# Kernel tuning notes

Measured on AMD Instinct MI355X. Metric: run time of the kernel, lower is better.

The kernel has to match this reference:

```python
import jax, jax.numpy as jnp
import numpy as np

M, N, D = 512, 4096, 128
H = N // D  # 32
L = 4096   # cache length


def setup_inputs() -> dict:
    key = jax.random.key(0)
    ks = jax.random.split(key, 6)
    s = 1.0 / np.sqrt(N)
    return {
        "X": jax.random.normal(ks[0], (M, N), jnp.float32),
        "W_q": jax.random.normal(ks[1], (N, N), jnp.float32) * s,
        "W_k": jax.random.normal(ks[2], (N, N), jnp.float32) * s,
        "W_v": jax.random.normal(ks[3], (N, N), jnp.float32) * s,
        "cache_K": jax.random.normal(ks[4], (H, L, D), jnp.float32),
        "cache_V": jax.random.normal(ks[5], (H, L, D), jnp.float32),
        "P": 3584,
    }


def reference(X, W_q, W_k, W_v, cache_K, cache_V, P):
    # nn.Linear(N, N, bias=False): y = x @ W.T
    q = (X @ W_q.T).reshape(M, H, D).transpose(1, 0, 2)  # [H, M, D]
    k = (X @ W_k.T).reshape(M, H, D).transpose(1, 0, 2)  # [H, M, D]
    v = (X @ W_v.T).reshape(M, H, D).transpose(1, 0, 2)  # [H, M, D]
    # KV-cache write at position P (static slice under jit for fixed P)
    cK = jax.lax.dynamic_update_slice(cache_K, k, (0, P, 0))  # [H, L, D]
    cV = jax.lax.dynamic_update_slice(cache_V, v, (0, P, 0))
    # attention over the full cache, no 1/sqrt(D) scaling (faithful to source)
    scores = jnp.einsum("hmd,hld->hml", q, cK)   # [H, M, L]
    weights = jax.nn.softmax(scores, axis=-1)
    out = jnp.einsum("hml,hld->hmd", weights, cV)  # [H, M, D]
    return out.transpose(1, 0, 2).reshape(M, H * D)  # [M, N]
```

## Files before the change

### kernel.cpp

```cpp
#include <hip/hip_runtime.h>
#include <hip/hip_fp16.h>

typedef _Float16 f16x8 __attribute__((ext_vector_type(8)));
typedef float    f32x4 __attribute__((ext_vector_type(4)));

#define MFMA16(a,b,c) __builtin_amdgcn_mfma_f32_16x16x32_f16(a,b,c,0,0,0)

__device__ __forceinline__ void gload_lds16(const void* g, void* l) {
  __builtin_amdgcn_global_load_lds(
      (const __attribute__((address_space(1))) void*)g,
      (__attribute__((address_space(3))) void*)l, 16, 0, 0);
}

__global__ void cvt_f32_f16(const float* __restrict__ src,
                            _Float16* __restrict__ dst, int n8) {
  int i = blockIdx.x * blockDim.x + threadIdx.x;
  int stride = gridDim.x * blockDim.x;
  for (; i < n8; i += stride) {
    const float4* s = (const float4*)src + 2 * (size_t)i;
    float4 a = s[0], b = s[1];
    f16x8 o;
    o[0]=(_Float16)a.x; o[1]=(_Float16)a.y; o[2]=(_Float16)a.z; o[3]=(_Float16)a.w;
    o[4]=(_Float16)b.x; o[5]=(_Float16)b.y; o[6]=(_Float16)b.z; o[7]=(_Float16)b.w;
    ((f16x8*)dst)[i] = o;
  }
}

__global__ __launch_bounds__(256) void cvt_transpose_v(const float* __restrict__ src,
                                                       _Float16* __restrict__ dst) {
  __shared__ _Float16 t[64][72];
  const int b = blockIdx.x;
  const int h = b >> 7, rest = b & 127;
  const int lt = rest >> 1, dt = rest & 1;
  const int l0 = lt * 64, d0 = dt * 64;
  const int tid = threadIdx.x;
  const int r = tid >> 4, c4 = (tid & 15) * 4;
#pragma unroll
  for (int i = 0; i < 4; i++) {
    int l = r + i * 16;
    float4 v = *(const float4*)&src[((size_t)h * 4096 + l0 + l) * 128 + d0 + c4];
    t[c4 + 0][l] = (_Float16)v.x;
    t[c4 + 1][l] = (_Float16)v.y;
    t[c4 + 2][l] = (_Float16)v.z;
    t[c4 + 3][l] = (_Float16)v.w;
  }
  __syncthreads();
  const int d = tid >> 2, lc = (tid & 3) * 16;
#pragma unroll
  for (int i = 0; i < 2; i++) {
    f16x8 o = *(const f16x8*)&t[d][lc + i * 8];
    *(f16x8*)&dst[((size_t)h * 128 + d0 + d) * 4096 + l0 + lc + i * 8] = o;
  }
}

__global__ __launch_bounds__(256, 3) void qkv_gemm(
    const _Float16* __restrict__ X,
    const float* __restrict__ Wq,
    const float* __restrict__ Wk,
    const float* __restrict__ Wv,
    _Float16* __restrict__ Q16,
    _Float16* __restrict__ Kc,
    _Float16* __restrict__ Vt16,
    const int* __restrict__ Pp)
{
  __shared__ __align__(16) _Float16 As[2 * 128 * 64];
  __shared__ __align__(16) _Float16 Bs[2 * 64 * 64];
  const int bid = blockIdx.x;
  const int xcd = bid & 7, s = bid >> 3;
  const int nt = xcd * 24 + (s >> 2);
  const int mt = s & 3;
  const int m0 = mt * 128, n0 = nt * 64;
  const int tid = threadIdx.x, wave = tid >> 6, lane = tid & 63;
  const int g = lane >> 4, c = lane & 15;
  const int wr = wave >> 1, wc = wave & 1;
  const float* Wp = (n0 < 4096) ? Wq : ((n0 < 8192) ? Wk : Wv);
  const int n0l = n0 & 4095;
  const int ar  = lane >> 3;
  const int acs = (lane & 7) * 16;
  const int brow = tid >> 2;
  const int bc32 = (tid & 3) * 16;
  const float* wsrc = Wp + (size_t)(n0l + brow) * 4096 + bc32;
  const int bsw = (brow & 7) << 4;

  float4 breg0, breg1, breg2, breg3;
  auto loadB = [&](int k0) {
    const float* ns = wsrc + k0;
    breg0 = *(const float4*)(ns);
    breg1 = *(const float4*)(ns + 4);
    breg2 = *(const float4*)(ns + 8);
    breg3 = *(const float4*)(ns + 12);
  };
  auto writeB = [&](int buf) {
    f16x8 h0, h1;
    h0[0]=(_Float16)breg0.x; h0[1]=(_Float16)breg0.y; h0[2]=(_Float16)breg0.z; h0[3]=(_Float16)breg0.w;
    h0[4]=(_Float16)breg1.x; h0[5]=(_Float16)breg1.y; h0[6]=(_Float16)breg1.z; h0[7]=(_Float16)breg1.w;
    h1[0]=(_Float16)breg2.x; h1[1]=(_Float16)breg2.y; h1[2]=(_Float16)breg2.z; h1[3]=(_Float16)breg2.w;
    h1[4]=(_Float16)breg3.x; h1[5]=(_Float16)breg3.y; h1[6]=(_Float16)breg3.z; h1[7]=(_Float16)breg3.w;
    char* rb = (char*)Bs + buf * 8192 + brow * 128;
    *(f16x8*)(rb + (((tid & 3) * 32)      ^ bsw)) = h0;
    *(f16x8*)(rb + (((tid & 3) * 32 + 16) ^ bsw)) = h1;
  };
  auto stageA = [&](int k0, int buf) {
#pragma unroll
    for (int p = 0; p < 4; p++) {
      int chunk = wave * 4 + p;
      int row = chunk * 8 + ar;
      gload_lds16((const char*)(X + (size_t)(m0 + row) * 4096 + k0) + (acs ^ ((row & 7) << 4)),
                  (char*)As + buf * 16384 + chunk * 1024);
    }
  };

  f32x4 acc[4][2] = {};
  loadB(0);
  writeB(0);
  stageA(0, 0);
  loadB(64);
  asm volatile("s_waitcnt vmcnt(4) lgkmcnt(0)" ::: "memory");
  __builtin_amdgcn_sched_barrier(0);
  __builtin_amdgcn_s_barrier();
  __builtin_amdgcn_sched_barrier(0);

  for (int t = 0; t < 64; ++t) {
    const int k0 = t << 6;
    const int cur = t & 1, nxt = cur ^ 1;
    stageA((k0 + 64) & 4095, nxt);
    const char* Ab = (const char*)As + cur * 16384;
    const char* Bb = (const char*)Bs + cur * 8192;
    f16x8 af[2][4], bf[2][2];
#pragma unroll
    for (int mi = 0; mi < 4; mi++) {
      int row = wr * 64 + mi * 16 + c;
      int sw = (row & 7) << 4;
#pragma unroll
      for (int kc = 0; kc < 2; kc++)
        af[kc][mi] = *(const f16x8*)(Ab + row * 128 + ((kc * 64 + g * 16) ^ sw));
    }
#pragma unroll
    for (int ni = 0; ni < 2; ni++) {
      int row = wc * 32 + ni * 16 + c;
      int sw = (row & 7) << 4;
#pragma unroll
      for (int kc = 0; kc < 2; kc++)
        bf[kc][ni] = *(const f16x8*)(Bb + row * 128 + ((kc * 64 + g * 16) ^ sw));
    }
    __builtin_amdgcn_s_setprio(1);
#pragma unroll
    for (int kc = 0; kc < 2; kc++)
#pragma unroll
      for (int mi = 0; mi < 4; mi++)
#pragma unroll
        for (int ni = 0; ni < 2; ni++)
          acc[mi][ni] = MFMA16(af[kc][mi], bf[kc][ni], acc[mi][ni]);
    __builtin_amdgcn_s_setprio(0);
    asm volatile("s_waitcnt vmcnt(4)" ::: "memory");
    writeB(nxt);
    loadB((k0 + 128) & 4095);
    asm volatile("s_waitcnt vmcnt(4) lgkmcnt(0)" ::: "memory");
    __builtin_amdgcn_sched_barrier(0);
    __builtin_amdgcn_s_barrier();
    __builtin_amdgcn_sched_barrier(0);
  }

  const int p = Pp[0];
  const int wsel = n0 >> 12;
  const int h = (n0 & 4095) >> 7;
  const int dbase = n0 & 127;
#pragma unroll
  for (int mi = 0; mi < 4; mi++) {
#pragma unroll
    for (int ni = 0; ni < 2; ni++) {
#pragma unroll
      for (int j = 0; j < 4; j++) {
        int m = m0 + wr * 64 + mi * 16 + 4 * g + j;
        int d = dbase + wc * 32 + ni * 16 + c;
        _Float16 hv = (_Float16)acc[mi][ni][j];
        if (wsel == 0)      Q16[(size_t)(h * 512 + m) * 128 + d] = hv;
        else if (wsel == 1) Kc[(size_t)(h * 4096 + p + m) * 128 + d] = hv;
        else                Vt16[((size_t)h * 128 + d) * 4096 + p + m] = hv;
      }
    }
  }
}

__global__ __launch_bounds__(512, 2) void attn_part(
    const _Float16* __restrict__ Q16,
    const _Float16* __restrict__ Kc,
    const _Float16* __restrict__ Vt,
    float* __restrict__ Opart,
    float* __restrict__ Mpart,
    float* __restrict__ Lpart)
{
  __shared__ __align__(16) _Float16 Ks[64 * 128];
  __shared__ __align__(16) _Float16 Vs[128 * 64];
  __shared__ __align__(16) _Float16 Pl[8][32][68];
  const int bid = blockIdx.x;
  const int xcd = bid & 7, s = bid >> 3;
  const int group = xcd * 16 + (s >> 1);
  const int mt = s & 1;
  const int ls = group >> 5, h = group & 31;
  const int m0 = mt * 256;
  const int tid = threadIdx.x, wave = tid >> 6, lane = tid & 63;
  const int g = lane >> 4, c = lane & 15;
  const int mw = m0 + wave * 32;
  const _Float16* Kh  = Kc + (size_t)h * 4096 * 128;
  const _Float16* Vth = Vt + (size_t)h * 128 * 4096;
  f16x8 qf[2][4];
#pragma unroll
  for (int mi = 0; mi < 2; mi++)
#pragma unroll
    for (int kc = 0; kc < 4; kc++)
      qf[mi][kc] = *(const f16x8*)&Q16[(size_t)(h * 512 + mw + mi * 16 + c) * 128 + kc * 32 + g * 8];
  f32x4 o[2][8] = {};
  float mrow[2][4], lrow[2][4];
#pragma unroll
  for (int mi = 0; mi < 2; mi++)
#pragma unroll
    for (int j = 0; j < 4; j++) { mrow[mi][j] = -3e38f; lrow[mi][j] = 0.f; }
  const int klr = lane >> 4, klb = (lane & 15) * 16;
  const int vlr = lane >> 3, vlb = (lane & 7) * 16;

  const int l_begin = ls * 1024;
  for (int l0 = l_begin; l0 < l_begin + 1024; l0 += 64) {
    __syncthreads();
#pragma unroll
    for (int p = 0; p < 2; p++) {
      int chunk = p * 8 + wave;
      int kr = chunk * 4 + klr;
      gload_lds16((const char*)Kh + (size_t)(l0 + kr) * 256 + (klb ^ ((kr & 7) << 4)),
                  (char*)Ks + chunk * 1024);
      int vd = chunk * 8 + vlr;
      gload_lds16((const char*)Vth + (size_t)vd * 8192 + (size_t)l0 * 2 + (vlb ^ ((vd & 7) << 4)),
                  (char*)Vs + chunk * 1024);
    }
    __syncthreads();
    f32x4 sc[2][4] = {};
#pragma unroll
    for (int ni = 0; ni < 4; ni++) {
      int kr = ni * 16 + c;
      f16x8 kf[4];
#pragma unroll
      for (int kc = 0; kc < 4; kc++)
        kf[kc] = *(const f16x8*)((const char*)Ks + kr * 256 + ((kc * 64 + g * 16) ^ ((kr & 7) << 4)));
#pragma unroll
      for (int mi = 0; mi < 2; mi++)
#pragma unroll
        for (int kc = 0; kc < 4; kc++)
          sc[mi][ni] = MFMA16(qf[mi][kc], kf[kc], sc[mi][ni]);
    }
#pragma unroll
    for (int mi = 0; mi < 2; mi++) {
      float scale[4];
#pragma unroll
      for (int j = 0; j < 4; j++) {
        float tm = sc[mi][0][j];
#pragma unroll
        for (int ni = 1; ni < 4; ni++) tm = fmaxf(tm, sc[mi][ni][j]);
        tm = fmaxf(tm, __shfl_xor(tm, 1, 64));
        tm = fmaxf(tm, __shfl_xor(tm, 2, 64));
        tm = fmaxf(tm, __shfl_xor(tm, 4, 64));
        tm = fmaxf(tm, __shfl_xor(tm, 8, 64));
        float mn = fmaxf(mrow[mi][j], tm);
        scale[j] = __expf(mrow[mi][j] - mn);
        mrow[mi][j] = mn;
      }
      float rs[4] = {0.f, 0.f, 0.f, 0.f};
#pragma unroll
      for (int ni = 0; ni < 4; ni++) {
#pragma unroll
        for (int j = 0; j < 4; j++) {
          float pv = __expf(sc[mi][ni][j] - mrow[mi][j]);
          sc[mi][ni][j] = pv;
          rs[j] += pv;
        }
      }
#pragma unroll
      for (int j = 0; j < 4; j++) {
        rs[j] += __shfl_xor(rs[j], 1, 64);
        rs[j] += __shfl_xor(rs[j], 2, 64);
        rs[j] += __shfl_xor(rs[j], 4, 64);
        rs[j] += __shfl_xor(rs[j], 8, 64);
        lrow[mi][j] = lrow[mi][j] * scale[j] + rs[j];
      }
#pragma unroll
      for (int dn = 0; dn < 8; dn++)
#pragma unroll
        for (int j = 0; j < 4; j++) o[mi][dn][j] *= scale[j];
#pragma unroll
      for (int ni = 0; ni < 4; ni++)
#pragma unroll
        for (int j = 0; j < 4; j++)
          Pl[wave][mi * 16 + 4 * g + j][ni * 16 + c] = (_Float16)sc[mi][ni][j];
    }
    f16x8 pa[2][2];
#pragma unroll
    for (int mi = 0; mi < 2; mi++)
#pragma unroll
      for (int kc = 0; kc < 2; kc++)
        pa[mi][kc] = *(const f16x8*)&Pl[wave][mi * 16 + c][kc * 32 + g * 8];
#pragma unroll
    for (int dn = 0; dn < 8; dn++) {
      int vr = dn * 16 + c;
#pragma unroll
      for (int kc = 0; kc < 2; kc++) {
        f16x8 vb = *(const f16x8*)((const char*)Vs + vr * 128 + ((kc * 64 + g * 16) ^ ((vr & 7) << 4)));
#pragma unroll
        for (int mi = 0; mi < 2; mi++)
          o[mi][dn] = MFMA16(pa[mi][kc], vb, o[mi][dn]);
      }
    }
  }
  const size_t pbase = ((size_t)(ls * 32 + h) * 512);
#pragma unroll
  for (int mi = 0; mi < 2; mi++) {
#pragma unroll
    for (int dn = 0; dn < 8; dn++) {
#pragma unroll
      for (int j = 0; j < 4; j++) {
        int m = mw + mi * 16 + 4 * g + j;
        Opart[(pbase + m) * 128 + dn * 16 + c] = o[mi][dn][j];
      }
    }
  }
  if (c == 0) {
#pragma unroll
    for (int mi = 0; mi < 2; mi++)
#pragma unroll
      for (int j = 0; j < 4; j++) {
        int m = mw + mi * 16 + 4 * g + j;
        Mpart[pbase + m] = mrow[mi][j];
        Lpart[pbase + m] = lrow[mi][j];
      }
  }
}

__global__ __launch_bounds__(256) void attn_combine(
    const float* __restrict__ Opart,
    const float* __restrict__ Mpart,
    const float* __restrict__ Lpart,
    float* __restrict__ out)
{
  int idx = blockIdx.x * 256 + threadIdx.x;
  int row = idx >> 5;
  int d4  = idx & 31;
  int h = row >> 9, m = row & 511;
  float Ms[4];
  float mx = -3e38f;
#pragma unroll
  for (int s = 0; s < 4; s++) {
    Ms[s] = Mpart[(size_t)(s * 32 + h) * 512 + m];
    mx = fmaxf(mx, Ms[s]);
  }
  float lsum = 0.f;
  float4 acc = make_float4(0.f, 0.f, 0.f, 0.f);
#pragma unroll
  for (int s = 0; s < 4; s++) {
    float w = __expf(Ms[s] - mx);
    lsum += w * Lpart[(size_t)(s * 32 + h) * 512 + m];
    float4 ov = ((const float4*)(Opart + ((size_t)(s * 32 + h) * 512 + m) * 128))[d4];
    acc.x += w * ov.x; acc.y += w * ov.y; acc.z += w * ov.z; acc.w += w * ov.w;
  }
  float inv = 1.f / lsum;
  float4 r = make_float4(acc.x * inv, acc.y * inv, acc.z * inv, acc.w * inv);
  *(float4*)&out[(size_t)m * 4096 + h * 128 + d4 * 4] = r;
}

extern "C" void kernel_launch(void* const* d_in, const int* in_sizes, int n_in,
                              void* d_out, int out_size, void* d_ws, size_t ws_size,
                              hipStream_t stream) {
  const float* X  = (const float*)d_in[0];
  const float* Wq = (const float*)d_in[1];
  const float* Wk = (const float*)d_in[2];
  const float* Wv = (const float*)d_in[3];
  const float* cK = (const float*)d_in[4];
  const float* cV = (const float*)d_in[5];
  const int*   Pp = (const int*)d_in[6];
  float* out = (float*)d_out;

  char* ws = (char*)d_ws;
  _Float16* X16  = (_Float16*)(ws);
  _Float16* Q16  = (_Float16*)(ws + ((size_t)100 << 20));
  _Float16* K16  = (_Float16*)(ws + ((size_t)104 << 20));
  _Float16* V16t = (_Float16*)(ws + ((size_t)136 << 20));
  float* Opart = (float*)(ws + ((size_t)4  << 20));
  float* Mpart = (float*)(ws + ((size_t)36 << 20));
  float* Lpart = (float*)(ws + ((size_t)37 << 20));

  const int NTH = 256;
  auto cvtl = [&](const float* s, _Float16* d, size_t n) {
    int n8 = (int)(n / 8);
    int grid = (n8 + NTH - 1) / NTH;
    if (grid > 2048) grid = 2048;
    cvt_f32_f16<<<dim3(grid), dim3(NTH), 0, stream>>>(s, d, n8);
  };
  cvtl(X,  X16, (size_t)512 * 4096);
  cvtl(cK, K16, (size_t)32 * 4096 * 128);
  cvt_transpose_v<<<dim3(4096), dim3(NTH), 0, stream>>>(cV, V16t);

  qkv_gemm<<<dim3(768), dim3(256), 0, stream>>>(X16, Wq, Wk, Wv, Q16, K16, V16t, Pp);
  attn_part<<<dim3(256), dim3(512), 0, stream>>>(Q16, K16, V16t, Opart, Mpart, Lpart);
  attn_combine<<<dim3(2048), dim3(256), 0, stream>>>(Opart, Mpart, Lpart, out);
}
```

Before: 239.1 us.

## Fuse KV-cache f32 conversion into attention loads and split L eight ways

Removes the separate full-cache f16 conversion and V transpose kernels. The attention kernel now reads fp32 cache_K/cache_V directly and converts them in registers, taking the freshly written f16 K/V only for tiles inside the updated window. It also moves to 1024-thread blocks covering all 512 rows, splits L into 8 chunks, and stores partial outputs in fp16. The QKV GEMM drops its hand-tuned waitcnt, setprio and barrier scheduling in favour of plain __syncthreads. The trade-offs are strided scalar V loads from fp32, lower fp16 precision in the partial outputs, and a possibly less overlapped GEMM pipeline.

```diff
diff --git a/kernel.cpp b/kernel.cpp
--- a/kernel.cpp
+++ b/kernel.cpp
@@ -2,6 +2,7 @@
 #include <hip/hip_fp16.h>
 
 typedef _Float16 f16x8 __attribute__((ext_vector_type(8)));
+typedef _Float16 f16x4 __attribute__((ext_vector_type(4)));
 typedef float    f32x4 __attribute__((ext_vector_type(4)));
 
 #define MFMA16(a,b,c) __builtin_amdgcn_mfma_f32_16x16x32_f16(a,b,c,0,0,0)
@@ -26,33 +27,6 @@
   }
 }
 
-__global__ __launch_bounds__(256) void cvt_transpose_v(const float* __restrict__ src,
-                                                       _Float16* __restrict__ dst) {
-  __shared__ _Float16 t[64][72];
-  const int b = blockIdx.x;
-  const int h = b >> 7, rest = b & 127;
-  const int lt = rest >> 1, dt = rest & 1;
-  const int l0 = lt * 64, d0 = dt * 64;
-  const int tid = threadIdx.x;
-  const int r = tid >> 4, c4 = (tid & 15) * 4;
-#pragma unroll
-  for (int i = 0; i < 4; i++) {
-    int l = r + i * 16;
-    float4 v = *(const float4*)&src[((size_t)h * 4096 + l0 + l) * 128 + d0 + c4];
-    t[c4 + 0][l] = (_Float16)v.x;
-    t[c4 + 1][l] = (_Float16)v.y;
-    t[c4 + 2][l] = (_Float16)v.z;
-    t[c4 + 3][l] = (_Float16)v.w;
-  }
-  __syncthreads();
-  const int d = tid >> 2, lc = (tid & 3) * 16;
-#pragma unroll
-  for (int i = 0; i < 2; i++) {
-    f16x8 o = *(const f16x8*)&t[d][lc + i * 8];
-    *(f16x8*)&dst[((size_t)h * 128 + d0 + d) * 4096 + l0 + lc + i * 8] = o;
-  }
-}
-
 __global__ __launch_bounds__(256, 3) void qkv_gemm(
     const _Float16* __restrict__ X,
     const float* __restrict__ Wq,
@@ -63,14 +37,16 @@
     _Float16* __restrict__ Vt16,
     const int* __restrict__ Pp)
 {
-  __shared__ __align__(16) _Float16 As[2 * 128 * 64];
-  __shared__ __align__(16) _Float16 Bs[2 * 64 * 64];
+  __shared__ __align__(16) _Float16 smem[2 * (128 + 64) * 64];
+  _Float16* As = smem;
+  _Float16* Bs = smem + 2 * 128 * 64;
   const int bid = blockIdx.x;
+  const int tid = threadIdx.x;
   const int xcd = bid & 7, s = bid >> 3;
   const int nt = xcd * 24 + (s >> 2);
   const int mt = s & 3;
   const int m0 = mt * 128, n0 = nt * 64;
-  const int tid = threadIdx.x, wave = tid >> 6, lane = tid & 63;
+  const int wave = tid >> 6, lane = tid & 63;
   const int g = lane >> 4, c = lane & 15;
   const int wr = wave >> 1, wc = wave & 1;
   const float* Wp = (n0 < 4096) ? Wq : ((n0 < 8192) ? Wk : Wv);
@@ -82,20 +58,17 @@
   const float* wsrc = Wp + (size_t)(n0l + brow) * 4096 + bc32;
   const int bsw = (brow & 7) << 4;
 
-  float4 breg0, breg1, breg2, breg3;
+  float4 breg[4];
   auto loadB = [&](int k0) {
     const float* ns = wsrc + k0;
-    breg0 = *(const float4*)(ns);
-    breg1 = *(const float4*)(ns + 4);
-    breg2 = *(const float4*)(ns + 8);
-    breg3 = *(const float4*)(ns + 12);
+#pragma unroll
+    for (int i = 0; i < 4; i++) breg[i] = *(const float4*)(ns + i * 4);
   };
   auto writeB = [&](int buf) {
+    const float* bv = (const float*)breg;
     f16x8 h0, h1;
-    h0[0]=(_Float16)breg0.x; h0[1]=(_Float16)breg0.y; h0[2]=(_Float16)breg0.z; h0[3]=(_Float16)breg0.w;
-    h0[4]=(_Float16)breg1.x; h0[5]=(_Float16)breg1.y; h0[6]=(_Float16)breg1.z; h0[7]=(_Float16)breg1.w;
-    h1[0]=(_Float16)breg2.x; h1[1]=(_Float16)breg2.y; h1[2]=(_Float16)breg2.z; h1[3]=(_Float16)breg2.w;
-    h1[4]=(_Float16)breg3.x; h1[5]=(_Float16)breg3.y; h1[6]=(_Float16)breg3.z; h1[7]=(_Float16)breg3.w;
+#pragma unroll
+    for (int i = 0; i < 8; i++) { h0[i] = (_Float16)bv[i]; h1[i] = (_Float16)bv[8 + i]; }
     char* rb = (char*)Bs + buf * 8192 + brow * 128;
     *(f16x8*)(rb + (((tid & 3) * 32)      ^ bsw)) = h0;
     *(f16x8*)(rb + (((tid & 3) * 32 + 16) ^ bsw)) = h1;
@@ -115,15 +88,13 @@
   writeB(0);
   stageA(0, 0);
   loadB(64);
-  asm volatile("s_waitcnt vmcnt(4) lgkmcnt(0)" ::: "memory");
-  __builtin_amdgcn_sched_barrier(0);
-  __builtin_amdgcn_s_barrier();
-  __builtin_amdgcn_sched_barrier(0);
+  __syncthreads();
 
   for (int t = 0; t < 64; ++t) {
-    const int k0 = t << 6;
     const int cur = t & 1, nxt = cur ^ 1;
-    stageA((k0 + 64) & 4095, nxt);
+    writeB(nxt);
+    loadB(((t + 2) & 63) << 6);
+    stageA(((t + 1) & 63) << 6, nxt);
     const char* Ab = (const char*)As + cur * 16384;
     const char* Bb = (const char*)Bs + cur * 8192;
     f16x8 af[2][4], bf[2][2];
@@ -143,7 +114,6 @@
       for (int kc = 0; kc < 2; kc++)
         bf[kc][ni] = *(const f16x8*)(Bb + row * 128 + ((kc * 64 + g * 16) ^ sw));
     }
-    __builtin_amdgcn_s_setprio(1);
 #pragma unroll
     for (int kc = 0; kc < 2; kc++)
 #pragma unroll
@@ -151,14 +121,7 @@
 #pragma unroll
         for (int ni = 0; ni < 2; ni++)
           acc[mi][ni] = MFMA16(af[kc][mi], bf[kc][ni], acc[mi][ni]);
-    __builtin_amdgcn_s_setprio(0);
-    asm volatile("s_waitcnt vmcnt(4)" ::: "memory");
-    writeB(nxt);
-    loadB((k0 + 128) & 4095);
-    asm volatile("s_waitcnt vmcnt(4) lgkmcnt(0)" ::: "memory");
-    __builtin_amdgcn_sched_barrier(0);
-    __builtin_amdgcn_s_barrier();
-    __builtin_amdgcn_sched_barrier(0);
+    __syncthreads();
   }
 
   const int p = Pp[0];
@@ -182,28 +145,30 @@
   }
 }
 
-__global__ __launch_bounds__(512, 2) void attn_part(
+__global__ __launch_bounds__(1024, 1) void attn_part(
     const _Float16* __restrict__ Q16,
-    const _Float16* __restrict__ Kc,
+    const _Float16* __restrict__ K16,
     const _Float16* __restrict__ Vt,
-    float* __restrict__ Opart,
+    const float* __restrict__ cK,
+    const float* __restrict__ cV,
+    _Float16* __restrict__ Opart,
     float* __restrict__ Mpart,
-    float* __restrict__ Lpart)
+    float* __restrict__ Lpart,
+    const int* __restrict__ Pp)
 {
   __shared__ __align__(16) _Float16 Ks[64 * 128];
   __shared__ __align__(16) _Float16 Vs[128 * 64];
-  __shared__ __align__(16) _Float16 Pl[8][32][68];
+  __shared__ __align__(16) _Float16 Pl[16][32][68];
   const int bid = blockIdx.x;
-  const int xcd = bid & 7, s = bid >> 3;
-  const int group = xcd * 16 + (s >> 1);
-  const int mt = s & 1;
-  const int ls = group >> 5, h = group & 31;
-  const int m0 = mt * 256;
+  const int ls = bid & 7, h = bid >> 3;
   const int tid = threadIdx.x, wave = tid >> 6, lane = tid & 63;
   const int g = lane >> 4, c = lane & 15;
-  const int mw = m0 + wave * 32;
-  const _Float16* Kh  = Kc + (size_t)h * 4096 * 128;
-  const _Float16* Vth = Vt + (size_t)h * 128 * 4096;
+  const int mw = wave * 32;
+  const int p = Pp[0];
+  const _Float16* K16h = K16 + (size_t)h * 4096 * 128;
+  const _Float16* Vth  = Vt  + (size_t)h * 128 * 4096;
+  const float* cKh = cK + (size_t)h * 4096 * 128;
+  const float* cVh = cV + (size_t)h * 4096 * 128;
   f16x8 qf[2][4];
 #pragma unroll
   for (int mi = 0; mi < 2; mi++)
@@ -216,31 +181,64 @@
   for (int mi = 0; mi < 2; mi++)
 #pragma unroll
     for (int j = 0; j < 4; j++) { mrow[mi][j] = -3e38f; lrow[mi][j] = 0.f; }
-  const int klr = lane >> 4, klb = (lane & 15) * 16;
-  const int vlr = lane >> 3, vlb = (lane & 7) * 16;
-
-  const int l_begin = ls * 1024;
-  for (int l0 = l_begin; l0 < l_begin + 1024; l0 += 64) {
+
+  const int kr = tid >> 4, kq = tid & 15;
+  const int ksw = (kr & 7) << 4;
+  const int vd = tid & 127, vlg = tid >> 7;
+  const int vsw = (vd & 7) << 4;
+  float4 ka0, ka1;
+  float vr8[8];
+  f16x8 vh16;
+  bool cur16 = false;
+
+  auto loadTile = [&](int l0) {
+    cur16 = ((unsigned)(l0 - p) < 512u);
+    if (!cur16) {
+      const float* ks = cKh + (size_t)(l0 + kr) * 128 + kq * 8;
+      ka0 = ((const float4*)ks)[0];
+      ka1 = ((const float4*)ks)[1];
+      const float* vs0 = cVh + (size_t)(l0 + vlg * 8) * 128 + vd;
+#pragma unroll
+      for (int i = 0; i < 8; i++) vr8[i] = vs0[(size_t)i * 128];
+    } else {
+      ka0 = *(const float4*)(K16h + (size_t)(l0 + kr) * 128 + kq * 8);
+      vh16 = *(const f16x8*)(Vth + (size_t)vd * 4096 + l0 + vlg * 8);
+    }
+  };
+  auto writeTile = [&]() {
+    f16x8 hk;
+    if (!cur16) {
+      hk[0]=(_Float16)ka0.x; hk[1]=(_Float16)ka0.y; hk[2]=(_Float16)ka0.z; hk[3]=(_Float16)ka0.w;
+      hk[4]=(_Float16)ka1.x; hk[5]=(_Float16)ka1.y; hk[6]=(_Float16)ka1.z; hk[7]=(_Float16)ka1.w;
+    } else {
+      hk = *(f16x8*)&ka0;
+    }
+    *(f16x8*)((char*)Ks + kr * 256 + ((kq * 16) ^ ksw)) = hk;
+    f16x8 hv;
+    if (!cur16) {
+#pragma unroll
+      for (int i = 0; i < 8; i++) hv[i] = (_Float16)vr8[i];
+    } else {
+      hv = vh16;
+    }
+    *(f16x8*)((char*)Vs + vd * 128 + ((vlg * 16) ^ vsw)) = hv;
+  };
+
+  const int l_begin = ls * 512;
+  loadTile(l_begin);
+  for (int l0 = l_begin; l0 < l_begin + 512; l0 += 64) {
     __syncthreads();
-#pragma unroll
-    for (int p = 0; p < 2; p++) {
-      int chunk = p * 8 + wave;
-      int kr = chunk * 4 + klr;
-      gload_lds16((const char*)Kh + (size_t)(l0 + kr) * 256 + (klb ^ ((kr & 7) << 4)),
-                  (char*)Ks + chunk * 1024);
-      int vd = chunk * 8 + vlr;
-      gload_lds16((const char*)Vth + (size_t)vd * 8192 + (size_t)l0 * 2 + (vlb ^ ((vd & 7) << 4)),
-                  (char*)Vs + chunk * 1024);
-    }
+    writeTile();
+    if (l0 + 64 < l_begin + 512) loadTile(l0 + 64);
     __syncthreads();
     f32x4 sc[2][4] = {};
 #pragma unroll
     for (int ni = 0; ni < 4; ni++) {
-      int kr = ni * 16 + c;
+      int krr = ni * 16 + c;
       f16x8 kf[4];
 #pragma unroll
       for (int kc = 0; kc < 4; kc++)
-        kf[kc] = *(const f16x8*)((const char*)Ks + kr * 256 + ((kc * 64 + g * 16) ^ ((kr & 7) << 4)));
+        kf[kc] = *(const f16x8*)((const char*)Ks + krr * 256 + ((kc * 64 + g * 16) ^ ((krr & 7) << 4)));
 #pragma unroll
       for (int mi = 0; mi < 2; mi++)
 #pragma unroll
@@ -299,10 +297,10 @@
         pa[mi][kc] = *(const f16x8*)&Pl[wave][mi * 16 + c][kc * 32 + g * 8];
 #pragma unroll
     for (int dn = 0; dn < 8; dn++) {
-      int vr = dn * 16 + c;
+      int vrr = dn * 16 + c;
 #pragma unroll
       for (int kc = 0; kc < 2; kc++) {
-        f16x8 vb = *(const f16x8*)((const char*)Vs + vr * 128 + ((kc * 64 + g * 16) ^ ((vr & 7) << 4)));
+        f16x8 vb = *(const f16x8*)((const char*)Vs + vrr * 128 + ((kc * 64 + g * 16) ^ ((vrr & 7) << 4)));
 #pragma unroll
         for (int mi = 0; mi < 2; mi++)
           o[mi][dn] = MFMA16(pa[mi][kc], vb, o[mi][dn]);
@@ -317,7 +315,7 @@
 #pragma unroll
       for (int j = 0; j < 4; j++) {
         int m = mw + mi * 16 + 4 * g + j;
-        Opart[(pbase + m) * 128 + dn * 16 + c] = o[mi][dn][j];
+        Opart[(pbase + m) * 128 + dn * 16 + c] = (_Float16)o[mi][dn][j];
       }
     }
   }
@@ -334,7 +332,7 @@
 }
 
 __global__ __launch_bounds__(256) void attn_combine(
-    const float* __restrict__ Opart,
+    const _Float16* __restrict__ Opart,
     const float* __restrict__ Mpart,
     const float* __restrict__ Lpart,
     float* __restrict__ out)
@@ -343,21 +341,22 @@
   int row = idx >> 5;
   int d4  = idx & 31;
   int h = row >> 9, m = row & 511;
-  float Ms[4];
+  float Ms[8];
   float mx = -3e38f;
 #pragma unroll
-  for (int s = 0; s < 4; s++) {
+  for (int s = 0; s < 8; s++) {
     Ms[s] = Mpart[(size_t)(s * 32 + h) * 512 + m];
     mx = fmaxf(mx, Ms[s]);
   }
   float lsum = 0.f;
   float4 acc = make_float4(0.f, 0.f, 0.f, 0.f);
 #pragma unroll
-  for (int s = 0; s < 4; s++) {
+  for (int s = 0; s < 8; s++) {
     float w = __expf(Ms[s] - mx);
     lsum += w * Lpart[(size_t)(s * 32 + h) * 512 + m];
-    float4 ov = ((const float4*)(Opart + ((size_t)(s * 32 + h) * 512 + m) * 128))[d4];
-    acc.x += w * ov.x; acc.y += w * ov.y; acc.z += w * ov.z; acc.w += w * ov.w;
+    f16x4 ov = *(const f16x4*)(Opart + ((size_t)(s * 32 + h) * 512 + m) * 128 + d4 * 4);
+    acc.x += w * (float)ov[0]; acc.y += w * (float)ov[1];
+    acc.z += w * (float)ov[2]; acc.w += w * (float)ov[3];
   }
   float inv = 1.f / lsum;
   float4 r = make_float4(acc.x * inv, acc.y * inv, acc.z * inv, acc.w * inv);
@@ -377,26 +376,17 @@
   float* out = (float*)d_out;
 
   char* ws = (char*)d_ws;
-  _Float16* X16  = (_Float16*)(ws);
+  _Float16* X16   = (_Float16*)(ws);
+  _Float16* Opart = (_Float16*)(ws + ((size_t)4  << 20));
+  float* Mpart = (float*)(ws + ((size_t)36 << 20));
+  float* Lpart = (float*)(ws + ((size_t)37 << 20));
   _Float16* Q16  = (_Float16*)(ws + ((size_t)100 << 20));
   _Float16* K16  = (_Float16*)(ws + ((size_t)104 << 20));
   _Float16* V16t = (_Float16*)(ws + ((size_t)136 << 20));
-  float* Opart = (float*)(ws + ((size_t)4  << 20));
-  float* Mpart = (float*)(ws + ((size_t)36 << 20));
-  float* Lpart = (float*)(ws + ((size_t)37 << 20));
-
-  const int NTH = 256;
-  auto cvtl = [&](const float* s, _Float16* d, size_t n) {
-    int n8 = (int)(n / 8);
-    int grid = (n8 + NTH - 1) / NTH;
-    if (grid > 2048) grid = 2048;
-    cvt_f32_f16<<<dim3(grid), dim3(NTH), 0, stream>>>(s, d, n8);
-  };
-  cvtl(X,  X16, (size_t)512 * 4096);
-  cvtl(cK, K16, (size_t)32 * 4096 * 128);
-  cvt_transpose_v<<<dim3(4096), dim3(NTH), 0, stream>>>(cV, V16t);
-
+
+  cvt_f32_f16<<<dim3(1024), dim3(256), 0, stream>>>(X, X16, 512 * 4096 / 8);
   qkv_gemm<<<dim3(768), dim3(256), 0, stream>>>(X16, Wq, Wk, Wv, Q16, K16, V16t, Pp);
-  attn_part<<<dim3(256), dim3(512), 0, stream>>>(Q16, K16, V16t, Opart, Mpart, Lpart);
+  attn_part<<<dim3(256), dim3(1024), 0, stream>>>(Q16, K16, V16t, cK, cV,
+                                                  Opart, Mpart, Lpart, Pp);
   attn_combine<<<dim3(2048), dim3(256), 0, stream>>>(Opart, Mpart, Lpart, out);
 }
```

Result: slower. 373.2 us (+56.1%).
